# Optimization experiments

Measured on AMD Instinct MI355X. Metric: run time of the kernel, lower is better.

## Reference

```python
import jax, jax.numpy as jnp
import numpy as np

N_NODES = 50000
N_EDGES = 600000
F_IN = 128
H_DIM = 256
N_CLASSES = 16
N_GRAPHS = 64


def _sage_conv(x, edge_index, W_l, W_r, b, num_nodes):
    # PyG SAGEConv (aggr='mean', root_weight=True):
    #   out = lin_l(mean_{j in N(i)} x_j) + lin_r(x_i)
    src, dst = edge_index[0], edge_index[1]
    msg_sum = jax.ops.segment_sum(x[src], dst, num_segments=num_nodes)      # [N, F]
    cnt = jax.ops.segment_sum(jnp.ones((edge_index.shape[1],), x.dtype), dst,
                              num_segments=num_nodes)                        # [N]
    mean = msg_sum / jnp.maximum(cnt, 1.0)[:, None]
    return mean @ W_l + x @ W_r + b


def _global_mean_pool(x, batch, num_graphs):
    s = jax.ops.segment_sum(x, batch, num_segments=num_graphs)               # [G, C]
    c = jax.ops.segment_sum(jnp.ones((x.shape[0],), x.dtype), batch,
                            num_segments=num_graphs)                         # [G]
    return s / jnp.maximum(c, 1.0)[:, None]


def setup_inputs() -> dict:
    key = jax.random.key(0)
    ks = jax.random.split(key, 9)
    x = jax.random.normal(ks[0], (N_NODES, F_IN), dtype=jnp.float32)
    edge_index = jax.random.randint(ks[1], (2, N_EDGES), 0, N_NODES)
    batch = jnp.sort(jax.random.randint(ks[2], (N_NODES,), 0, N_GRAPHS))
    # SAGEConv params (glorot-ish scale)
    def w(k, fi, fo):
        return jax.random.normal(k, (fi, fo), dtype=jnp.float32) / np.sqrt(fi)
    return {
        "x": x,
        "edge_index": edge_index,
        "batch": batch,
        "W1_l": w(ks[3], F_IN, H_DIM),
        "W1_r": w(ks[4], F_IN, H_DIM),
        "b1": jnp.zeros((H_DIM,), jnp.float32),
        "W2_l": w(ks[5], H_DIM, N_CLASSES),
        "W2_r": w(ks[6], H_DIM, N_CLASSES),
        "b2": jnp.zeros((N_CLASSES,), jnp.float32),
    }


def reference(x, edge_index, batch, W1_l, W1_r, b1, W2_l, W2_r, b2):
    n = x.shape[0]
    h = _sage_conv(x, edge_index, W1_l, W1_r, b1, n)
    h = jax.nn.relu(h)
    h = _sage_conv(h, edge_index, W2_l, W2_r, b2, n)
    h = jax.nn.relu(h)
    g = _global_mean_pool(h, batch, N_GRAPHS)
    return jax.nn.log_softmax(g, axis=1)
```

## Files before the change

### kernel.cpp

```cpp
#include <hip/hip_runtime.h>

#define N_NODES   50000
#define N_EDGES   600000
#define F_IN      128
#define H_DIM     256
#define N_CLASSES 16
#define N_GRAPHS  64
#define M_PAD     50048

typedef unsigned short ushort_t;
typedef unsigned int   uint_t;
typedef __attribute__((ext_vector_type(8))) short bf16x8;
typedef __attribute__((ext_vector_type(4))) float f32x4;

__device__ inline ushort_t f2bf(float f) {
    union { float f; uint_t u; } v; v.f = f;
    uint_t r = v.u + 0x7FFF + ((v.u >> 16) & 1);
    return (ushort_t)(r >> 16);
}
__device__ inline float bf2f(uint_t u) {
    union { uint_t u; float f; } v; v.u = u << 16;
    return v.f;
}
__device__ inline void load_lds16(const void* g, void* l) {
    __builtin_amdgcn_global_load_lds(
        (const __attribute__((address_space(1))) void*)g,
        (__attribute__((address_space(3))) void*)l, 16, 0, 0);
}

__global__ void hist_kernel(const int* __restrict__ dst, int* __restrict__ deg) {
    int e = blockIdx.x * blockDim.x + threadIdx.x;
    if (e < N_EDGES) atomicAdd(&deg[dst[e]], 1);
}

__global__ __launch_bounds__(256) void scan1_kernel(const int* __restrict__ deg,
                                                    int* __restrict__ bsum) {
    __shared__ int sc[256];
    const int t = threadIdx.x;
    const int i = blockIdx.x * 256 + t;
    sc[t] = (i < N_NODES) ? deg[i] : 0;
    __syncthreads();
    for (int s = 128; s > 0; s >>= 1) {
        if (t < s) sc[t] += sc[t + s];
        __syncthreads();
    }
    if (t == 0) bsum[blockIdx.x] = sc[0];
}

__global__ __launch_bounds__(256) void scan2_kernel(int* __restrict__ bsum, int nb) {
    __shared__ int sc[256];
    const int t = threadIdx.x;
    const int v = (t < nb) ? bsum[t] : 0;
    sc[t] = v;
    __syncthreads();
    for (int s = 1; s < 256; s <<= 1) {
        int add = (t >= s) ? sc[t - s] : 0;
        __syncthreads();
        sc[t] += add;
        __syncthreads();
    }
    if (t < nb) bsum[t] = sc[t] - v;
}

__global__ __launch_bounds__(256) void scan3_kernel(const int* __restrict__ deg,
                                                    const int* __restrict__ bsum,
                                                    int* __restrict__ off,
                                                    int* __restrict__ cursor) {
    __shared__ int sc[256];
    const int t = threadIdx.x;
    const int i = blockIdx.x * 256 + t;
    const int d = (i < N_NODES) ? deg[i] : 0;
    sc[t] = d;
    __syncthreads();
    for (int s = 1; s < 256; s <<= 1) {
        int add = (t >= s) ? sc[t - s] : 0;
        __syncthreads();
        sc[t] += add;
        __syncthreads();
    }
    if (i < N_NODES) {
        const int o = bsum[blockIdx.x] + sc[t] - d;
        off[i] = o;
        cursor[i] = o;
    }
    if (i == N_NODES) off[i] = N_EDGES;
}

__global__ void scatter_ids_kernel(const int* __restrict__ src,
                                   const int* __restrict__ dst,
                                   int* __restrict__ cursor,
                                   int* __restrict__ ssrc) {
    int e = blockIdx.x * blockDim.x + threadIdx.x;
    if (e >= N_EDGES) return;
    int pos = atomicAdd(&cursor[dst[e]], 1);
    ssrc[pos] = src[e];
}

__global__ void xcopy_kernel(const float* __restrict__ x, ushort_t* __restrict__ ha) {
    int t = blockIdx.x * blockDim.x + threadIdx.x;
    if (t >= N_NODES * 32) return;
    int n = t >> 5, c = t & 31;
    const float4 v = *reinterpret_cast<const float4*>(x + (size_t)n * F_IN + c * 4);
    uint2 pk;
    pk.x = (uint_t)f2bf(v.x) | ((uint_t)f2bf(v.y) << 16);
    pk.y = (uint_t)f2bf(v.z) | ((uint_t)f2bf(v.w) << 16);
    *reinterpret_cast<uint2*>(ha + (size_t)n * 256 + 128 + c * 4) = pk;
}

__global__ __launch_bounds__(256) void agg1_kernel(const int* __restrict__ off,
                                                   const int* __restrict__ ssrc,
                                                   ushort_t* __restrict__ ha,
                                                   float* __restrict__ invdeg) {
    const int n = blockIdx.x * 4 + (threadIdx.x >> 6);
    if (n >= N_NODES) return;
    const int lane = threadIdx.x & 63;
    const int half = lane >> 5;
    const int c = lane & 31;
    const int o0 = off[n], o1 = off[n + 1];
    float a0 = 0.f, a1 = 0.f, a2 = 0.f, a3 = 0.f;
    for (int e = o0 + half; e < o1; e += 2) {
        const int s = ssrc[e];
        const uint2 v = *reinterpret_cast<const uint2*>(ha + (size_t)s * 256 + 128 + c * 4);
        a0 += bf2f(v.x & 0xFFFFu);
        a1 += bf2f(v.x >> 16);
        a2 += bf2f(v.y & 0xFFFFu);
        a3 += bf2f(v.y >> 16);
    }
    a0 += __shfl_xor(a0, 32);
    a1 += __shfl_xor(a1, 32);
    a2 += __shfl_xor(a2, 32);
    a3 += __shfl_xor(a3, 32);
    const float iv = 1.0f / fmaxf((float)(o1 - o0), 1.0f);
    if (half == 0) {
        uint2 pk;
        pk.x = (uint_t)f2bf(a0 * iv) | ((uint_t)f2bf(a1 * iv) << 16);
        pk.y = (uint_t)f2bf(a2 * iv) | ((uint_t)f2bf(a3 * iv) << 16);
        *reinterpret_cast<uint2*>(ha + (size_t)n * 256 + c * 4) = pk;
        if (c == 0) invdeg[n] = iv;
    }
}

__global__ __launch_bounds__(256) void btprep_kernel(
    const float* __restrict__ W1l, const float* __restrict__ W1r,
    const float* __restrict__ W2l, const float* __restrict__ W2r,
    ushort_t* __restrict__ Bt, ushort_t* __restrict__ Bt2) {
    const int bi = blockIdx.x;
    const int k = threadIdx.x;
    if (bi < 256) {
        const float v = (k < 128) ? W1l[k * H_DIM + bi] : W1r[(k - 128) * H_DIM + bi];
        Bt[bi * 256 + k] = f2bf(v);
    } else {
        const int c = bi - 256;
        const float v = (c < 16) ? W2l[k * N_CLASSES + c] : W2r[k * N_CLASSES + (c - 16)];
        Bt2[c * 256 + k] = f2bf(v);
    }
}

__global__ __launch_bounds__(256) void gemm1_fused_kernel(
    const ushort_t* __restrict__ ha, const ushort_t* __restrict__ Bt,
    const ushort_t* __restrict__ Bt2, const float* __restrict__ b1,
    float* __restrict__ p, float* __restrict__ r) {
    __shared__ ushort_t sA[64 * 256];
    __shared__ ushort_t sB[64 * 256];
    const int tid  = threadIdx.x;
    const int mblk = blockIdx.x;

    const char* gA = (const char*)ha + (size_t)mblk * 32768;
    const char* gB = (const char*)Bt;
#pragma unroll
    for (int i = 0; i < 8; ++i) {
        const int d = (i * 256 + tid) * 16;
        const int s = d ^ (((d >> 9) & 7) << 4);
        load_lds16(gA + s, (char*)sA + (d & ~1023));
    }
#pragma unroll
    for (int i = 0; i < 8; ++i) {
        const int d = (i * 256 + tid) * 16;
        const int s = d ^ (((d >> 9) & 7) << 4);
        load_lds16(gB + s, (char*)sB + (d & ~1023));
    }
    __syncthreads();

    const int w    = tid >> 6;
    const int lane = tid & 63;
    const int lr   = lane & 15;
    const int hi   = lane >> 4;
    const int m0   = w * 16;

    bf16x8 afr[8];
    {
        const int row = m0 + lr;
        const int sw = (row & 7) << 4;
#pragma unroll
        for (int ks = 0; ks < 8; ++ks)
            afr[ks] = *reinterpret_cast<const bf16x8*>(
                (const char*)sA + ((row * 512 + ks * 64 + hi * 16) ^ sw));
    }

    f32x4 acc[16];
#pragma unroll
    for (int t = 0; t < 16; ++t) acc[t] = (f32x4){0.f, 0.f, 0.f, 0.f};

#pragma unroll
    for (int ph = 0; ph < 4; ++ph) {
#pragma unroll
        for (int fnl = 0; fnl < 4; ++fnl) {
            const int rn = fnl * 16 + lr;
            const int sw = (rn & 7) << 4;
#pragma unroll
            for (int ks = 0; ks < 8; ++ks) {
                const bf16x8 bfr = *reinterpret_cast<const bf16x8*>(
                    (const char*)sB + ((rn * 512 + ks * 64 + hi * 16) ^ sw));
                acc[ph * 4 + fnl] = __builtin_amdgcn_mfma_f32_16x16x32_bf16(
                    afr[ks], bfr, acc[ph * 4 + fnl], 0, 0, 0);
            }
        }
        __syncthreads();
        if (ph < 3) {
#pragma unroll
            for (int i = 0; i < 8; ++i) {
                const int d = (i * 256 + tid) * 16;
                const int s = d ^ (((d >> 9) & 7) << 4);
                load_lds16(gB + (ph + 1) * 32768 + s, (char*)sB + (d & ~1023));
            }
            __syncthreads();
        }
    }

#pragma unroll
    for (int t = 0; t < 16; ++t) {
        const int colG = t * 16 + lr;
        const float bias = b1[colG];
#pragma unroll
        for (int i = 0; i < 4; ++i) {
            const int row = m0 + hi * 4 + i;
            const float h = fmaxf(acc[t][i] + bias, 0.f);
            const int ad = (row * 512 + colG * 2) ^ ((row & 7) << 4);
            *reinterpret_cast<ushort_t*>((char*)sB + ad) = f2bf(h);
        }
    }
    __syncthreads();

    const char* bt2b = (const char*)Bt2;
    const int nr = m0 + lr;
    const int swn = (nr & 7) << 4;
    f32x4 acc2[2] = {(f32x4){0.f, 0.f, 0.f, 0.f}, (f32x4){0.f, 0.f, 0.f, 0.f}};
#pragma unroll
    for (int fc = 0; fc < 2; ++fc) {
#pragma unroll
        for (int k2 = 0; k2 < 8; ++k2) {
            const bf16x8 a2 = *reinterpret_cast<const bf16x8*>(
                bt2b + (fc * 16 + lr) * 512 + k2 * 64 + hi * 16);
            const bf16x8 b2 = *reinterpret_cast<const bf16x8*>(
                (const char*)sB + ((nr * 512 + k2 * 64 + hi * 16) ^ swn));
            acc2[fc] = __builtin_amdgcn_mfma_f32_16x16x32_bf16(a2, b2, acc2[fc], 0, 0, 0);
        }
    }

    const int node = mblk * 64 + nr;
    if (node < N_NODES) {
#pragma unroll
        for (int i = 0; i < 4; ++i) {
            p[(size_t)node * N_CLASSES + hi * 4 + i] = acc2[0][i];
            r[(size_t)node * N_CLASSES + hi * 4 + i] = acc2[1][i];
        }
    }
}

__global__ __launch_bounds__(256) void agg2_kernel(const float* __restrict__ p,
                                                   const int* __restrict__ off,
                                                   const int* __restrict__ ssrc,
                                                   float* __restrict__ psum) {
    const int n = blockIdx.x * 16 + (threadIdx.x >> 4);
    if (n >= N_NODES) return;
    const int c = threadIdx.x & 15;
    const int o0 = off[n], o1 = off[n + 1];
    float acc = 0.f;
    for (int e = o0; e < o1; ++e)
        acc += p[(size_t)ssrc[e] * N_CLASSES + c];
    psum[(size_t)n * N_CLASSES + c] = acc;
}

__global__ __launch_bounds__(256) void pool_kernel(
    const float* __restrict__ psum, const float* __restrict__ r,
    const float* __restrict__ invdeg, const float* __restrict__ b2,
    const int* __restrict__ batch,
    float* __restrict__ gsum, float* __restrict__ gcnt) {
    __shared__ float lgsum[N_GRAPHS * N_CLASSES];
    __shared__ float lgcnt[N_GRAPHS];
    __shared__ int gminmax[2];
    const int t = threadIdx.x;
    const int base = blockIdx.x * 64;
#pragma unroll
    for (int k = 0; k < 4; ++k) lgsum[t + 256 * k] = 0.f;
    if (t < N_GRAPHS) lgcnt[t] = 0.f;
    if (t == 0) {
        gminmax[0] = batch[base];
        int last = base + 63; if (last >= N_NODES) last = N_NODES - 1;
        gminmax[1] = batch[last];
    }
    __syncthreads();

    const int j = t & 15;
    const float bj = b2[j];
#pragma unroll
    for (int k = 0; k < 4; ++k) {
        const int i = base + (t >> 4) + 16 * k;
        if (i < N_NODES) {
            float h = psum[(size_t)i * N_CLASSES + j] * invdeg[i]
                      + r[(size_t)i * N_CLASSES + j] + bj;
            h = fmaxf(h, 0.f);
            const int g = batch[i];
            atomicAdd(&lgsum[g * N_CLASSES + j], h);
            if (j == 0) atomicAdd(&lgcnt[g], 1.0f);
        }
    }
    __syncthreads();

    const int gmin = gminmax[0], gmax = gminmax[1];
    for (int gg = gmin + (t >> 4); gg <= gmax; gg += 16) {
        const float v = lgsum[gg * N_CLASSES + j];
        if (v != 0.f) atomicAdd(&gsum[gg * N_CLASSES + j], v);
    }
    if (t < N_GRAPHS) {
        const int gg = gmin + t;
        if (gg <= gmax) {
            const float c = lgcnt[gg];
            if (c != 0.f) atomicAdd(&gcnt[gg], c);
        }
    }
}

__global__ void lsm_kernel(const float* __restrict__ gsum,
                           const float* __restrict__ gcnt,
                           float* __restrict__ out) {
    int g = threadIdx.x;
    if (g >= N_GRAPHS) return;
    const float iv = 1.0f / fmaxf(gcnt[g], 1.0f);
    float v[N_CLASSES];
    float m = -1e30f;
#pragma unroll
    for (int j = 0; j < N_CLASSES; ++j) {
        v[j] = gsum[g * N_CLASSES + j] * iv;
        m = fmaxf(m, v[j]);
    }
    float s = 0.f;
#pragma unroll
    for (int j = 0; j < N_CLASSES; ++j) s += expf(v[j] - m);
    const float lse = logf(s);
#pragma unroll
    for (int j = 0; j < N_CLASSES; ++j) out[g * N_CLASSES + j] = v[j] - m - lse;
}

extern "C" void kernel_launch(void* const* d_in, const int* in_sizes, int n_in,
                              void* d_out, int out_size, void* d_ws, size_t ws_size,
                              hipStream_t stream) {
    const float* x    = (const float*)d_in[0];
    const int*   ei   = (const int*)d_in[1];
    const int*   batch= (const int*)d_in[2];
    const float* W1l  = (const float*)d_in[3];
    const float* W1r  = (const float*)d_in[4];
    const float* b1   = (const float*)d_in[5];
    const float* W2l  = (const float*)d_in[6];
    const float* W2r  = (const float*)d_in[7];
    const float* b2   = (const float*)d_in[8];
    float* out = (float*)d_out;

    const int* src = ei;
    const int* dst = ei + N_EDGES;

    float* ws     = (float*)d_ws;
    int*   deg    = (int*)ws;
    float* invdeg = ws;
    float* gsum   = ws + 50000;
    float* gcnt   = gsum + 1024;
    int*   off    = (int*)(gcnt + 64);
    int*   cursor = off + 50004;
    int*   ssrc   = cursor + 50000;
    int*   bsum   = ssrc + 600000;
    ushort_t* Bt  = (ushort_t*)(bsum + 256);
    ushort_t* Bt2 = Bt + 65536;
    ushort_t* ha  = Bt2 + 8192;
    float* p      = (float*)(ha + (size_t)M_PAD * 256);
    float* r      = p + 800000;
    float* psum   = (float*)ha;

    const size_t zero_elems = 50000 + 1024 + 64;
    hipMemsetAsync(ws, 0, zero_elems * sizeof(float), stream);

    const int NB = (N_NODES + 255) / 256;
    hist_kernel<<<(N_EDGES + 255) / 256, 256, 0, stream>>>(dst, deg);
    scan1_kernel<<<NB, 256, 0, stream>>>(deg, bsum);
    scan2_kernel<<<1, 256, 0, stream>>>(bsum, NB);
    scan3_kernel<<<NB, 256, 0, stream>>>(deg, bsum, off, cursor);
    scatter_ids_kernel<<<(N_EDGES + 255) / 256, 256, 0, stream>>>(src, dst, cursor, ssrc);
    xcopy_kernel<<<(N_NODES * 32 + 255) / 256, 256, 0, stream>>>(x, ha);
    agg1_kernel<<<(N_NODES + 3) / 4, 256, 0, stream>>>(off, ssrc, ha, invdeg);
    btprep_kernel<<<288, 256, 0, stream>>>(W1l, W1r, W2l, W2r, Bt, Bt2);
    gemm1_fused_kernel<<<M_PAD / 64, 256, 0, stream>>>(ha, Bt, Bt2, b1, p, r);
    agg2_kernel<<<(N_NODES + 15) / 16, 256, 0, stream>>>(p, off, ssrc, psum);
    pool_kernel<<<(N_NODES + 63) / 64, 256, 0, stream>>>(psum, r, invdeg, b2, batch, gsum, gcnt);
    lsm_kernel<<<1, 64, 0, stream>>>(gsum, gcnt, out);
}
```

Baseline: 185.7 us.

## Widen gather loads and spread edges across more lanes in both aggregation kernels

agg1 now uses 16-byte loads with 16 lanes per row and 4 edge slots per wave, then reduces across the slots with shuffles. agg2 moves from one node per 16 threads walking edges serially to one node per wave, with float4 loads over 16 edge slots and a shuffle reduction. The goal is more memory-level parallelism on the irregular gathers, since average degree is about 12. The hipMemsetAsync is also replaced by a small zero kernel to cut the launch cost of the memset. The price is shuffle-reduction overhead and idle lanes on low-degree nodes, and agg2 now launches four times as many blocks.

```diff
diff --git a/kernel.cpp b/kernel.cpp
--- a/kernel.cpp
+++ b/kernel.cpp
@@ -26,6 +26,11 @@
     __builtin_amdgcn_global_load_lds(
         (const __attribute__((address_space(1))) void*)g,
         (__attribute__((address_space(3))) void*)l, 16, 0, 0);
+}
+
+__global__ void zero_kernel(uint_t* __restrict__ w, int n) {
+    int i = blockIdx.x * blockDim.x + threadIdx.x;
+    if (i < n) w[i] = 0u;
 }
 
 __global__ void hist_kernel(const int* __restrict__ dst, int* __restrict__ deg) {
@@ -114,28 +119,31 @@
     const int n = blockIdx.x * 4 + (threadIdx.x >> 6);
     if (n >= N_NODES) return;
     const int lane = threadIdx.x & 63;
-    const int half = lane >> 5;
-    const int c = lane & 31;
+    const int slot = lane >> 4;
+    const int c    = lane & 15;
     const int o0 = off[n], o1 = off[n + 1];
-    float a0 = 0.f, a1 = 0.f, a2 = 0.f, a3 = 0.f;
-    for (int e = o0 + half; e < o1; e += 2) {
+    float a[8] = {0.f, 0.f, 0.f, 0.f, 0.f, 0.f, 0.f, 0.f};
+    for (int e = o0 + slot; e < o1; e += 4) {
         const int s = ssrc[e];
-        const uint2 v = *reinterpret_cast<const uint2*>(ha + (size_t)s * 256 + 128 + c * 4);
-        a0 += bf2f(v.x & 0xFFFFu);
-        a1 += bf2f(v.x >> 16);
-        a2 += bf2f(v.y & 0xFFFFu);
-        a3 += bf2f(v.y >> 16);
-    }
-    a0 += __shfl_xor(a0, 32);
-    a1 += __shfl_xor(a1, 32);
-    a2 += __shfl_xor(a2, 32);
-    a3 += __shfl_xor(a3, 32);
+        const uint4 v = *reinterpret_cast<const uint4*>(ha + (size_t)s * 256 + 128 + c * 8);
+        a[0] += bf2f(v.x & 0xFFFFu); a[1] += bf2f(v.x >> 16);
+        a[2] += bf2f(v.y & 0xFFFFu); a[3] += bf2f(v.y >> 16);
+        a[4] += bf2f(v.z & 0xFFFFu); a[5] += bf2f(v.z >> 16);
+        a[6] += bf2f(v.w & 0xFFFFu); a[7] += bf2f(v.w >> 16);
+    }
+#pragma unroll
+    for (int i = 0; i < 8; ++i) {
+        a[i] += __shfl_xor(a[i], 16);
+        a[i] += __shfl_xor(a[i], 32);
+    }
     const float iv = 1.0f / fmaxf((float)(o1 - o0), 1.0f);
-    if (half == 0) {
-        uint2 pk;
-        pk.x = (uint_t)f2bf(a0 * iv) | ((uint_t)f2bf(a1 * iv) << 16);
-        pk.y = (uint_t)f2bf(a2 * iv) | ((uint_t)f2bf(a3 * iv) << 16);
-        *reinterpret_cast<uint2*>(ha + (size_t)n * 256 + c * 4) = pk;
+    if (slot == 0) {
+        uint4 pk;
+        pk.x = (uint_t)f2bf(a[0] * iv) | ((uint_t)f2bf(a[1] * iv) << 16);
+        pk.y = (uint_t)f2bf(a[2] * iv) | ((uint_t)f2bf(a[3] * iv) << 16);
+        pk.z = (uint_t)f2bf(a[4] * iv) | ((uint_t)f2bf(a[5] * iv) << 16);
+        pk.w = (uint_t)f2bf(a[6] * iv) | ((uint_t)f2bf(a[7] * iv) << 16);
+        *reinterpret_cast<uint4*>(ha + (size_t)n * 256 + c * 8) = pk;
         if (c == 0) invdeg[n] = iv;
     }
 }
@@ -271,14 +279,27 @@
                                                    const int* __restrict__ off,
                                                    const int* __restrict__ ssrc,
                                                    float* __restrict__ psum) {
-    const int n = blockIdx.x * 16 + (threadIdx.x >> 4);
+    const int n = blockIdx.x * 4 + (threadIdx.x >> 6);
     if (n >= N_NODES) return;
-    const int c = threadIdx.x & 15;
+    const int lane = threadIdx.x & 63;
+    const int slot = lane >> 2;
+    const int c    = lane & 3;
     const int o0 = off[n], o1 = off[n + 1];
-    float acc = 0.f;
-    for (int e = o0; e < o1; ++e)
-        acc += p[(size_t)ssrc[e] * N_CLASSES + c];
-    psum[(size_t)n * N_CLASSES + c] = acc;
+    float4 acc = {0.f, 0.f, 0.f, 0.f};
+    for (int e = o0 + slot; e < o1; e += 16) {
+        const int s = ssrc[e];
+        const float4 v = *reinterpret_cast<const float4*>(p + (size_t)s * N_CLASSES + c * 4);
+        acc.x += v.x; acc.y += v.y; acc.z += v.z; acc.w += v.w;
+    }
+#pragma unroll
+    for (int o = 4; o < 64; o <<= 1) {
+        acc.x += __shfl_xor(acc.x, o);
+        acc.y += __shfl_xor(acc.y, o);
+        acc.z += __shfl_xor(acc.z, o);
+        acc.w += __shfl_xor(acc.w, o);
+    }
+    if (slot == 0)
+        *reinterpret_cast<float4*>(psum + (size_t)n * N_CLASSES + c * 4) = acc;
 }
 
 __global__ __launch_bounds__(256) void pool_kernel(
@@ -385,8 +406,8 @@
     float* r      = p + 800000;
     float* psum   = (float*)ha;
 
-    const size_t zero_elems = 50000 + 1024 + 64;
-    hipMemsetAsync(ws, 0, zero_elems * sizeof(float), stream);
+    const int zero_elems = 50000 + 1024 + 64;
+    zero_kernel<<<(zero_elems + 255) / 256, 256, 0, stream>>>((uint_t*)ws, zero_elems);
 
     const int NB = (N_NODES + 255) / 256;
     hist_kernel<<<(N_EDGES + 255) / 256, 256, 0, stream>>>(dst, deg);
@@ -398,7 +419,7 @@
     agg1_kernel<<<(N_NODES + 3) / 4, 256, 0, stream>>>(off, ssrc, ha, invdeg);
     btprep_kernel<<<288, 256, 0, stream>>>(W1l, W1r, W2l, W2r, Bt, Bt2);
     gemm1_fused_kernel<<<M_PAD / 64, 256, 0, stream>>>(ha, Bt, Bt2, b1, p, r);
-    agg2_kernel<<<(N_NODES + 15) / 16, 256, 0, stream>>>(p, off, ssrc, psum);
+    agg2_kernel<<<(N_NODES + 3) / 4, 256, 0, stream>>>(p, off, ssrc, psum);
     pool_kernel<<<(N_NODES + 63) / 64, 256, 0, stream>>>(psum, r, invdeg, b2, batch, gsum, gcnt);
     lsm_kernel<<<1, 64, 0, stream>>>(gsum, gcnt, out);
 }
```

New measurement: 171.1 us. 7.9% less time.
